# Optimization experiments

Measured on AMD Instinct MI355X. Metric: run time of the kernel, lower is better.

Reference implementation:

```python
import jax, jax.numpy as jnp
import numpy as np

BATCH = 32
ROW_DIM = 8192
COL_DIM = 8192
N_BLOCKS = 512
ROW_BS = ROW_DIM // N_BLOCKS  # 16
COL_BS = COL_DIM // N_BLOCKS  # 16


def setup_inputs() -> dict:
    key = jax.random.key(0)
    k1, k2 = jax.random.split(key)
    x = jax.random.normal(k1, (BATCH, COL_DIM), dtype=jnp.float32)
    # xavier-uniform-ish init scale for blocks [n_blocks, p, q]
    limit = np.sqrt(6.0 / (ROW_BS + COL_BS))
    blocks = jax.random.uniform(k2, (N_BLOCKS, ROW_BS, COL_BS), dtype=jnp.float32,
                                minval=-limit, maxval=limit)
    return {"x": x, "blocks": blocks}


def reference(x, blocks):
    b = x.shape[0]
    n, p, q = blocks.shape
    x_blocks = x.reshape(b, n, q)  # [B, n, q]
    # circulant index pattern: block (i, j) uses blocks[(i - j) % n]
    idx = (jnp.arange(n)[:, None] - jnp.arange(n)[None, :]) % n  # [n, n]
    blocks_shifted = blocks[idx]  # [n, n, p, q] -- the gather-expand intermediate
    y_blocks = jnp.einsum('mnpq,bnq->bmp', blocks_shifted, x_blocks)  # [B, n, p]
    return y_blocks.reshape(b, n * p)
```

## Files before the change

### kernel.cpp

```cpp
#include <hip/hip_runtime.h>
#include <hip/hip_bf16.h>

#define DIM 8192
#define KSPLIT 16
#define PARTIAL_ELEMS (32 * DIM)

typedef __bf16 bf16x8 __attribute__((ext_vector_type(8)));
typedef float f32x16 __attribute__((ext_vector_type(16)));

__device__ __forceinline__ unsigned short f2bf(float f) {
  union { float f; unsigned u; } v; v.f = f;
  unsigned r = v.u + 0x7FFFu + ((v.u >> 16) & 1u);
  return (unsigned short)(r >> 16);
}

__global__ __launch_bounds__(256, 2)
void bcl_mfma_kernel(const float* __restrict__ X,
                     const float* __restrict__ Blk,
                     float* __restrict__ Ws) {
  __shared__ __align__(16) unsigned short A_lds[64 * 32 * 8];
  __shared__ __align__(16) unsigned short B_lds[47 * 16 * 24];

  const int tid = threadIdx.x;
  const int mc  = blockIdx.x & 31;
  const int kc  = blockIdx.x >> 5;
  const int kbase = kc * 512;

  #pragma unroll
  for (int it = 0; it < 16; ++it) {
    const int i = tid + it * 256;
    const int L = i << 2;
    const int oct = L >> 8;
    const int r   = (L >> 3) & 31;
    const int j   = L & 7;
    const float4 v = *reinterpret_cast<const float4*>(X + r * DIM + kbase + oct * 8 + j);
    ushort4 s;
    s.x = f2bf(v.x); s.y = f2bf(v.y); s.z = f2bf(v.z); s.w = f2bf(v.w);
    *reinterpret_cast<ushort4*>(&A_lds[L]) = s;
  }

  const int dbase = (mc * 16 - kc * 32 - 31 + 512) & 511;
  for (int i = tid; i < 47 * 64; i += 256) {
    const int w = i >> 6;
    const int e = (i & 63) << 2;
    const int d = (dbase + w) & 511;
    const float4 v = *reinterpret_cast<const float4*>(Blk + d * 256 + e);
    ushort4 s;
    s.x = f2bf(v.x); s.y = f2bf(v.y); s.z = f2bf(v.z); s.w = f2bf(v.w);
    *reinterpret_cast<ushort4*>(&B_lds[w * 384 + (e >> 4) * 24 + (e & 15)]) = s;
  }

  __syncthreads();

  const int lane = tid & 63;
  const int wid  = tid >> 6;
  const int h    = lane >> 5;
  const int r31  = lane & 31;
  const int p    = lane & 15;
  const int msub = (lane >> 4) & 1;

  const unsigned short* Ab = &A_lds[(h * 32 + r31) * 8];
  const unsigned short* Bb = &B_lds[p * 24 + h * 8];
  const int wt0 = (wid * 2 + 0) * 2 + msub + 31;
  const int wt1 = wt0 + 2;

  f32x16 acc0, acc1;
  #pragma unroll
  for (int i = 0; i < 16; ++i) { acc0[i] = 0.0f; acc1[i] = 0.0f; }

  #pragma unroll 4
  for (int s = 0; s < 32; ++s) {
    const bf16x8 a  = *reinterpret_cast<const bf16x8*>(Ab + s * 512);
    const bf16x8 b0 = *reinterpret_cast<const bf16x8*>(Bb + (wt0 - s) * 384);
    const bf16x8 b1 = *reinterpret_cast<const bf16x8*>(Bb + (wt1 - s) * 384);
    acc0 = __builtin_amdgcn_mfma_f32_32x32x16_bf16(a, b0, acc0, 0, 0, 0);
    acc1 = __builtin_amdgcn_mfma_f32_32x32x16_bf16(a, b1, acc1, 0, 0, 0);
  }

  float* o0 = Ws + (size_t)kc * PARTIAL_ELEMS + mc * 256 + wid * 64 + r31;
  #pragma unroll
  for (int reg = 0; reg < 16; ++reg) {
    const int row = (reg & 3) + 8 * (reg >> 2) + 4 * h;
    o0[row * DIM]      = acc0[reg];
    o0[row * DIM + 32] = acc1[reg];
  }
}

__global__ __launch_bounds__(256)
void bcl_reduce_kernel(const float4* __restrict__ Ws, float4* __restrict__ Out) {
  const int f = blockIdx.x * 256 + threadIdx.x;
  float4 a = Ws[f];
  #pragma unroll
  for (int kc = 1; kc < KSPLIT; ++kc) {
    const float4 v = Ws[kc * (PARTIAL_ELEMS / 4) + f];
    a.x += v.x; a.y += v.y; a.z += v.z; a.w += v.w;
  }
  Out[f] = a;
}

extern "C" void kernel_launch(void* const* d_in, const int* in_sizes, int n_in,
                              void* d_out, int out_size, void* d_ws, size_t ws_size,
                              hipStream_t stream) {
  const float* X   = (const float*)d_in[0];
  const float* Blk = (const float*)d_in[1];
  float* Ws  = (float*)d_ws;
  float* Out = (float*)d_out;
  bcl_mfma_kernel<<<dim3(512), dim3(256), 0, stream>>>(X, Blk, Ws);
  bcl_reduce_kernel<<<dim3(PARTIAL_ELEMS / 4 / 256), dim3(256), 0, stream>>>(
      (const float4*)Ws, (float4*)Out);
}
```

Baseline: 73.41 us.

## Switch block-circulant matmul from 32x32x16 to 16x16x32 MFMA tiles

Replaces the 32x32x16 bf16 MFMA formulation with 16x16x32 MFMAs. X and the circulant weight blocks are staged in LDS with new layouts matching the new operand fragments, and each wave now holds eight 4-wide accumulators over half as many k-steps. The aim is a better operand fit for the 16x16 block structure and less padding in the weight LDS buffer. In exchange, the output stores are scattered differently and the k-loop issues more, smaller MFMA instructions.

```diff
diff --git a/kernel.cpp b/kernel.cpp
--- a/kernel.cpp
+++ b/kernel.cpp
@@ -6,7 +6,7 @@
 #define PARTIAL_ELEMS (32 * DIM)
 
 typedef __bf16 bf16x8 __attribute__((ext_vector_type(8)));
-typedef float f32x16 __attribute__((ext_vector_type(16)));
+typedef float f32x4 __attribute__((ext_vector_type(4)));
 
 __device__ __forceinline__ unsigned short f2bf(float f) {
   union { float f; unsigned u; } v; v.f = f;
@@ -18,8 +18,8 @@
 void bcl_mfma_kernel(const float* __restrict__ X,
                      const float* __restrict__ Blk,
                      float* __restrict__ Ws) {
-  __shared__ __align__(16) unsigned short A_lds[64 * 32 * 8];
-  __shared__ __align__(16) unsigned short B_lds[47 * 16 * 24];
+  __shared__ __align__(16) unsigned short Xl[16384];
+  __shared__ __align__(16) unsigned short Wl[47 * 256];
 
   const int tid = threadIdx.x;
   const int mc  = blockIdx.x & 31;
@@ -28,61 +28,73 @@
 
   #pragma unroll
   for (int it = 0; it < 16; ++it) {
-    const int i = tid + it * 256;
-    const int L = i << 2;
-    const int oct = L >> 8;
-    const int r   = (L >> 3) & 31;
-    const int j   = L & 7;
-    const float4 v = *reinterpret_cast<const float4*>(X + r * DIM + kbase + oct * 8 + j);
-    ushort4 s;
-    s.x = f2bf(v.x); s.y = f2bf(v.y); s.z = f2bf(v.z); s.w = f2bf(v.w);
-    *reinterpret_cast<ushort4*>(&A_lds[L]) = s;
+    const int L  = (tid + it * 256) << 2;
+    const int j4 = L & 7;
+    const int p  = (L >> 3) & 15;
+    const int kh = (L >> 7) & 3;
+    const int b0 = (L >> 9) & 1;
+    const int s  = (L >> 10) & 15;
+    const int batch = b0 * 16 + p;
+    const int kg = kbase + s * 32 + (kh >> 1) * 16 + (kh & 1) * 8 + j4;
+    const float4 v = *reinterpret_cast<const float4*>(X + batch * DIM + kg);
+    ushort4 u;
+    u.x = f2bf(v.x); u.y = f2bf(v.y); u.z = f2bf(v.z); u.w = f2bf(v.w);
+    *reinterpret_cast<ushort4*>(&Xl[L]) = u;
   }
 
-  const int dbase = (mc * 16 - kc * 32 - 31 + 512) & 511;
+  const int dbase = (mc * 16 - kc * 32 - 31) & 511;
   for (int i = tid; i < 47 * 64; i += 256) {
-    const int w = i >> 6;
-    const int e = (i & 63) << 2;
-    const int d = (dbase + w) & 511;
-    const float4 v = *reinterpret_cast<const float4*>(Blk + d * 256 + e);
-    ushort4 s;
-    s.x = f2bf(v.x); s.y = f2bf(v.y); s.z = f2bf(v.z); s.w = f2bf(v.w);
-    *reinterpret_cast<ushort4*>(&B_lds[w * 384 + (e >> 4) * 24 + (e & 15)]) = s;
+    const int w  = i >> 6;
+    const int r  = (i & 63) << 2;
+    const int qh = r >> 7;
+    const int p  = (r >> 3) & 15;
+    const int j4 = r & 7;
+    const int d  = (dbase + w) & 511;
+    const float4 v = *reinterpret_cast<const float4*>(Blk + d * 256 + p * 16 + qh * 8 + j4);
+    ushort4 u;
+    u.x = f2bf(v.x); u.y = f2bf(v.y); u.z = f2bf(v.z); u.w = f2bf(v.w);
+    *reinterpret_cast<ushort4*>(&Wl[w * 256 + r]) = u;
   }
 
   __syncthreads();
 
   const int lane = tid & 63;
   const int wid  = tid >> 6;
-  const int h    = lane >> 5;
-  const int r31  = lane & 31;
-  const int p    = lane & 15;
-  const int msub = (lane >> 4) & 1;
 
-  const unsigned short* Ab = &A_lds[(h * 32 + r31) * 8];
-  const unsigned short* Bb = &B_lds[p * 24 + h * 8];
-  const int wt0 = (wid * 2 + 0) * 2 + msub + 31;
-  const int wt1 = wt0 + 2;
+  const unsigned short* Xb = &Xl[lane << 3];
+  const unsigned short* Wb = &Wl[(((lane >> 5) ^ 1) << 8) + (((lane >> 4) & 1) << 7) + ((lane & 15) << 3)];
 
-  f32x16 acc0, acc1;
+  f32x4 acc[4][2];
   #pragma unroll
-  for (int i = 0; i < 16; ++i) { acc0[i] = 0.0f; acc1[i] = 0.0f; }
+  for (int t = 0; t < 4; ++t)
+    #pragma unroll
+    for (int b = 0; b < 2; ++b)
+      acc[t][b] = (f32x4){0.f, 0.f, 0.f, 0.f};
 
   #pragma unroll 4
-  for (int s = 0; s < 32; ++s) {
-    const bf16x8 a  = *reinterpret_cast<const bf16x8*>(Ab + s * 512);
-    const bf16x8 b0 = *reinterpret_cast<const bf16x8*>(Bb + (wt0 - s) * 384);
-    const bf16x8 b1 = *reinterpret_cast<const bf16x8*>(Bb + (wt1 - s) * 384);
-    acc0 = __builtin_amdgcn_mfma_f32_32x32x16_bf16(a, b0, acc0, 0, 0, 0);
-    acc1 = __builtin_amdgcn_mfma_f32_32x32x16_bf16(a, b1, acc1, 0, 0, 0);
+  for (int s = 0; s < 16; ++s) {
+    const bf16x8 x0 = *reinterpret_cast<const bf16x8*>(Xb + (s << 10));
+    const bf16x8 x1 = *reinterpret_cast<const bf16x8*>(Xb + (s << 10) + 512);
+    #pragma unroll
+    for (int t = 0; t < 4; ++t) {
+      const int mt = (wid << 2) + t;
+      const bf16x8 wf = *reinterpret_cast<const bf16x8*>(Wb + ((mt + 30 - 2 * s) << 8));
+      acc[t][0] = __builtin_amdgcn_mfma_f32_16x16x32_bf16(x0, wf, acc[t][0], 0, 0, 0);
+      acc[t][1] = __builtin_amdgcn_mfma_f32_16x16x32_bf16(x1, wf, acc[t][1], 0, 0, 0);
+    }
   }
 
-  float* o0 = Ws + (size_t)kc * PARTIAL_ELEMS + mc * 256 + wid * 64 + r31;
+  float* base = Ws + (size_t)kc * PARTIAL_ELEMS + mc * 256;
   #pragma unroll
-  for (int reg = 0; reg < 16; ++reg) {
-    const int row = (reg & 3) + 8 * (reg >> 2) + 4 * h;
-    o0[row * DIM]      = acc0[reg];
-    o0[row * DIM + 32] = acc1[reg];
+  for (int t = 0; t < 4; ++t) {
+    const int col = ((wid << 2) + t) * 16 + (lane & 15);
+    #pragma unroll
+    for (int b0 = 0; b0 < 2; ++b0) {
+      const int brow = b0 * 16 + ((lane >> 4) << 2);
+      #pragma unroll
+      for (int r = 0; r < 4; ++r)
+        base[(brow + r) * DIM + col] = acc[t][b0][r];
+    }
   }
 }
 
```

Measured after the change: 73.39 us, median of 2. About the same (-0.0%).
